# Kernel optimization log

Measured on AMD Instinct MI355X. Metric: run time of the kernel, lower is better.

Reference implementation:

```python
import jax, jax.numpy as jnp
import numpy as np

P = 7            # POOL_SIZE
NUM_CLASSES = 20
STRIDE = 16      # FEATURE_STRIDE
SCALE = 1.0 / STRIDE
C_IN = 512
C_MID = 2 * C_IN
C_CLS = P * P * (NUM_CLASSES + 1)        # 1029
C_BOX = P * P * (NUM_CLASSES + 1) * 4    # 4116
H, W = 38, 50
K = 300
IMG_H, IMG_W = 600.0, 800.0


def conv1x1(w, b, x):
    # w: [Cout, Cin], b: [Cout], x: [Cin, H, W] -> ReLU(conv) (CNNBlock = Conv2d 1x1 + ReLU)
    return jax.nn.relu(jnp.einsum('oi,ihw->ohw', w, x) + b[:, None, None])


def ps_roi_pool(maps, rois_xyxy):
    # maps: [Ctot, H, W] with Ctot = Cout*P*P, channel index = (c*P + ph)*P + pw
    # rois_xyxy: [K, 4] (x1, y1, x2, y2) in image coords. torchvision PSRoIPool math.
    Ctot, h, w = maps.shape
    Cout = Ctot // (P * P)
    x1 = jnp.round(rois_xyxy[:, 0]) * SCALE
    y1 = jnp.round(rois_xyxy[:, 1]) * SCALE
    x2 = (jnp.round(rois_xyxy[:, 2]) + 1.0) * SCALE
    y2 = (jnp.round(rois_xyxy[:, 3]) + 1.0) * SCALE
    roi_w = jnp.maximum(x2 - x1, 0.1)
    roi_h = jnp.maximum(y2 - y1, 0.1)
    bin_w = roi_w / P
    bin_h = roi_h / P
    i = jnp.arange(P, dtype=maps.dtype)
    hs = jnp.clip(jnp.floor(y1[:, None] + bin_h[:, None] * i), 0.0, h)        # [K,P]
    he = jnp.clip(jnp.ceil(y1[:, None] + bin_h[:, None] * (i + 1.0)), 0.0, h)
    ws = jnp.clip(jnp.floor(x1[:, None] + bin_w[:, None] * i), 0.0, w)
    we = jnp.clip(jnp.ceil(x1[:, None] + bin_w[:, None] * (i + 1.0)), 0.0, w)
    hidx = jnp.arange(h, dtype=maps.dtype)
    widx = jnp.arange(w, dtype=maps.dtype)
    hmask = ((hidx >= hs[..., None]) & (hidx < he[..., None])).astype(maps.dtype)  # [K,P,H]
    wmask = ((widx >= ws[..., None]) & (widx < we[..., None])).astype(maps.dtype)  # [K,P,W]
    maps_r = maps.reshape(Cout, P, P, h, w)
    t = jnp.einsum('cijhw,kih->kcijw', maps_r, hmask)     # reduce over h
    s = jnp.einsum('kcijw,kjw->kcij', t, wmask)           # reduce over w -> [K,Cout,P,P]
    cnt = ((he - hs)[:, :, None] * (we - ws)[:, None, :])[:, None]  # [K,1,P,P]
    return jnp.where(cnt > 0, s / jnp.maximum(cnt, 1.0), 0.0)


def setup_inputs() -> dict:
    key = jax.random.key(0)
    ks = jax.random.split(key, 10)
    feature = jax.random.normal(ks[0], (C_IN, H, W), dtype=jnp.float32)
    # rois in (y1, x1, y2, x2) image coords, matching the column permute in forward
    ymin = jax.random.uniform(ks[1], (K,), minval=0.0, maxval=IMG_H - 32.0)
    xmin = jax.random.uniform(ks[2], (K,), minval=0.0, maxval=IMG_W - 32.0)
    yh = jax.random.uniform(ks[3], (K,), minval=16.0, maxval=256.0)
    xw = jax.random.uniform(ks[4], (K,), minval=16.0, maxval=256.0)
    ymax = jnp.minimum(ymin + yh, IMG_H - 1.0)
    xmax = jnp.minimum(xmin + xw, IMG_W - 1.0)
    rois = jnp.stack([ymin, xmin, ymax, xmax], axis=1)
    sd1 = 1.0 / np.sqrt(C_IN)
    sd2 = 1.0 / np.sqrt(C_MID)
    w_double = jax.random.normal(ks[5], (C_MID, C_IN), dtype=jnp.float32) * sd1
    b_double = jnp.zeros((C_MID,), dtype=jnp.float32)
    w_score = jax.random.normal(ks[6], (C_CLS, C_MID), dtype=jnp.float32) * sd2
    b_score = jnp.zeros((C_CLS,), dtype=jnp.float32)
    w_bbox = jax.random.normal(ks[7], (C_BOX, C_MID), dtype=jnp.float32) * sd2
    b_bbox = jnp.zeros((C_BOX,), dtype=jnp.float32)
    return {"feature": feature, "rois": rois,
            "w_double": w_double, "b_double": b_double,
            "w_score": w_score, "b_score": b_score,
            "w_bbox": w_bbox, "b_bbox": b_bbox}


def reference(feature, rois, w_double, b_double, w_score, b_score, w_bbox, b_bbox):
    feat2 = conv1x1(w_double, b_double, feature)               # [2C, H, W]
    # rois given as (y1,x1,y2,x2) -> (x1,y1,x2,y2), per xy_indices_and_rois permute
    rois_xyxy = rois[:, jnp.array([1, 0, 3, 2])]
    score_maps = conv1x1(w_score, b_score, feat2)              # [P*P*(NC+1), H, W]
    class_vote = ps_roi_pool(score_maps, rois_xyxy)            # [K, NC+1, P, P]
    predicted_roi_score = jnp.mean(class_vote, axis=(-2, -1))  # AvgPool2d(P) + squeeze -> [K, NC+1]
    bbox_maps = conv1x1(w_bbox, b_bbox, feat2)                 # [P*P*(NC+1)*4, H, W]
    bbox_vote = ps_roi_pool(bbox_maps, rois_xyxy)              # [K, 4*(NC+1), P, P]
    predicted_roi_offset = jnp.mean(bbox_vote, axis=(-2, -1))  # [K, 4*(NC+1)]
    return predicted_roi_score, predicted_roi_offset
```

## Files before the change

kernel.cpp:

```cpp
#include <hip/hip_runtime.h>
#include <hip/hip_bf16.h>

#define P 7
#define C_IN 512
#define C_MID 1024
#define C_CLS 1029
#define C_BOX 4116
#define FH 38
#define FW 50
#define NPIX 1900
#define KROIS 300
#define COUT_SCORE 21
#define COUT_BOX 84
#define NPAIRS (KROIS * (COUT_SCORE + COUT_BOX))

#define LDP 40

__device__ float g_featT [NPIX * C_IN];
__device__ float g_feat2T[NPIX * C_MID];
__device__ float g_score [C_CLS * NPIX];
__device__ float g_bbox  [C_BOX * NPIX];

typedef __attribute__((ext_vector_type(8))) short bf16x8;
typedef __attribute__((ext_vector_type(4))) float f32x4;

__device__ __forceinline__ unsigned short f2b(float x) {
    unsigned u = __float_as_uint(x);
    unsigned r = u + 0x7fffu + ((u >> 16) & 1u);
    return (unsigned short)(r >> 16);
}
__device__ __forceinline__ float b2f(unsigned short h) {
    return __uint_as_float((unsigned)h << 16);
}

__device__ __forceinline__ void split16(const float4* v,
                                        unsigned short* dsth, unsigned short* dstl) {
    unsigned hu[8], lu[8];
    #pragma unroll
    for (int q = 0; q < 4; ++q) {
        const float a0 = v[q].x, a1 = v[q].y, a2 = v[q].z, a3 = v[q].w;
        const unsigned short h0 = f2b(a0), h1 = f2b(a1), h2 = f2b(a2), h3 = f2b(a3);
        const unsigned short l0 = f2b(a0 - b2f(h0)), l1 = f2b(a1 - b2f(h1));
        const unsigned short l2 = f2b(a2 - b2f(h2)), l3 = f2b(a3 - b2f(h3));
        hu[q * 2 + 0] = (unsigned)h0 | ((unsigned)h1 << 16);
        hu[q * 2 + 1] = (unsigned)h2 | ((unsigned)h3 << 16);
        lu[q * 2 + 0] = (unsigned)l0 | ((unsigned)l1 << 16);
        lu[q * 2 + 1] = (unsigned)l2 | ((unsigned)l3 << 16);
    }
    reinterpret_cast<uint4*>(dsth)[0] = make_uint4(hu[0], hu[1], hu[2], hu[3]);
    reinterpret_cast<uint4*>(dsth)[1] = make_uint4(hu[4], hu[5], hu[6], hu[7]);
    reinterpret_cast<uint4*>(dstl)[0] = make_uint4(lu[0], lu[1], lu[2], lu[3]);
    reinterpret_cast<uint4*>(dstl)[1] = make_uint4(lu[4], lu[5], lu[6], lu[7]);
}

__global__ __launch_bounds__(256) void transpose_k(const float* __restrict__ in)
{
    __shared__ float t[32][33];
    const int n0 = blockIdx.x * 32;
    const int k0 = blockIdx.y * 32;
    const int tx = threadIdx.x & 31;
    const int ty = threadIdx.x >> 5;
    #pragma unroll
    for (int j = 0; j < 4; ++j) {
        const int kk = k0 + ty + j * 8;
        const int nn = n0 + tx;
        t[ty + j * 8][tx] = (nn < NPIX) ? in[kk * NPIX + nn] : 0.f;
    }
    __syncthreads();
    #pragma unroll
    for (int j = 0; j < 4; ++j) {
        const int nn = n0 + ty + j * 8;
        const int kk = k0 + tx;
        if (nn < NPIX) g_featT[(size_t)nn * C_IN + kk] = t[tx][ty + j * 8];
    }
}

template <bool TROUT>
__global__ __launch_bounds__(256) void gemm_mfma(
    const float* __restrict__ W, const float* __restrict__ X,
    const float* __restrict__ bias, float* __restrict__ out,
    int M, int K, int N)
{
    __shared__ unsigned short sAh[128 * LDP], sAl[128 * LDP];
    __shared__ unsigned short sBh[128 * LDP], sBl[128 * LDP];

    const int tid = threadIdx.x;
    const int bm = blockIdx.y * 128;
    const int bn = blockIdx.x * 128;
    const int lane = tid & 63;
    const int wid = tid >> 6;
    const int wr = (wid >> 1) * 64;
    const int wc = (wid & 1) * 64;
    const int ll  = lane & 15;
    const int lh8 = (lane >> 4) * 8;
    const int lh4 = (lane >> 4) * 4;

    const int srow  = tid >> 1;
    const int skseg = (tid & 1) * 16;
    const int arow = bm + srow;
    const int brow = bn + srow;

    f32x4 acc[4][4];
    #pragma unroll
    for (int i = 0; i < 4; ++i)
        #pragma unroll
        for (int j = 0; j < 4; ++j) {
            f32x4 z = {0.f, 0.f, 0.f, 0.f};
            acc[i][j] = z;
        }

    float4 wa[4], wb[4];
    const float4 f4z = make_float4(0.f, 0.f, 0.f, 0.f);

    {
        const float* pa = W + (size_t)arow * K + skseg;
        if (arow < M) { wa[0] = ((const float4*)pa)[0]; wa[1] = ((const float4*)pa)[1];
                        wa[2] = ((const float4*)pa)[2]; wa[3] = ((const float4*)pa)[3]; }
        else          { wa[0] = wa[1] = wa[2] = wa[3] = f4z; }
        const float* pb = X + (size_t)brow * K + skseg;
        if (brow < N) { wb[0] = ((const float4*)pb)[0]; wb[1] = ((const float4*)pb)[1];
                        wb[2] = ((const float4*)pb)[2]; wb[3] = ((const float4*)pb)[3]; }
        else          { wb[0] = wb[1] = wb[2] = wb[3] = f4z; }
    }

    for (int k0 = 0; k0 < K; k0 += 32) {
        split16(wa, &sAh[srow * LDP + skseg], &sAl[srow * LDP + skseg]);
        split16(wb, &sBh[srow * LDP + skseg], &sBl[srow * LDP + skseg]);
        __syncthreads();

        const int kn = k0 + 32;
        if (kn < K) {
            const float* pa = W + (size_t)arow * K + kn + skseg;
            if (arow < M) { wa[0] = ((const float4*)pa)[0]; wa[1] = ((const float4*)pa)[1];
                            wa[2] = ((const float4*)pa)[2]; wa[3] = ((const float4*)pa)[3]; }
            const float* pb = X + (size_t)brow * K + kn + skseg;
            if (brow < N) { wb[0] = ((const float4*)pb)[0]; wb[1] = ((const float4*)pb)[1];
                            wb[2] = ((const float4*)pb)[2]; wb[3] = ((const float4*)pb)[3]; }
        }

        bf16x8 bhf[4], blf[4];
        #pragma unroll
        for (int nt = 0; nt < 4; ++nt) {
            const int r = wc + nt * 16 + ll;
            bhf[nt] = *reinterpret_cast<const bf16x8*>(&sBh[r * LDP + lh8]);
            blf[nt] = *reinterpret_cast<const bf16x8*>(&sBl[r * LDP + lh8]);
        }
        #pragma unroll
        for (int mt = 0; mt < 4; ++mt) {
            const int r = wr + mt * 16 + ll;
            const bf16x8 ahf = *reinterpret_cast<const bf16x8*>(&sAh[r * LDP + lh8]);
            const bf16x8 alf = *reinterpret_cast<const bf16x8*>(&sAl[r * LDP + lh8]);
            #pragma unroll
            for (int nt = 0; nt < 4; ++nt) {
                acc[mt][nt] = __builtin_amdgcn_mfma_f32_16x16x32_bf16(ahf, bhf[nt], acc[mt][nt], 0, 0, 0);
                acc[mt][nt] = __builtin_amdgcn_mfma_f32_16x16x32_bf16(ahf, blf[nt], acc[mt][nt], 0, 0, 0);
                acc[mt][nt] = __builtin_amdgcn_mfma_f32_16x16x32_bf16(alf, bhf[nt], acc[mt][nt], 0, 0, 0);
            }
        }
        __syncthreads();
    }

    #pragma unroll
    for (int mt = 0; mt < 4; ++mt) {
        #pragma unroll
        for (int nt = 0; nt < 4; ++nt) {
            const int m0 = bm + wr + mt * 16 + lh4;
            const int n  = bn + wc + nt * 16 + ll;
            if (TROUT) {
                if (n < N) {
                    float4 o;
                    o.x = fmaxf(acc[mt][nt][0] + bias[m0 + 0], 0.f);
                    o.y = fmaxf(acc[mt][nt][1] + bias[m0 + 1], 0.f);
                    o.z = fmaxf(acc[mt][nt][2] + bias[m0 + 2], 0.f);
                    o.w = fmaxf(acc[mt][nt][3] + bias[m0 + 3], 0.f);
                    *reinterpret_cast<float4*>(&out[(size_t)n * M + m0]) = o;
                }
            } else {
                #pragma unroll
                for (int r = 0; r < 4; ++r) {
                    const int m = m0 + r;
                    if (m < M && n < N)
                        out[(size_t)m * N + n] = fmaxf(acc[mt][nt][r] + bias[m], 0.f);
                }
            }
        }
    }
}

__global__ __launch_bounds__(256) void psroi_pool_mean(
    const float* __restrict__ rois, float* __restrict__ out)
{
    __shared__ float red[4][64];
    const int wid = threadIdx.x >> 6;
    const int lane = threadIdx.x & 63;
    const int pair = blockIdx.x * 4 + wid;

    const int k = pair / (COUT_SCORE + COUT_BOX);
    const int c = pair % (COUT_SCORE + COUT_BOX);

    const float* maps;
    int cbase;
    float* outp;
    if (c < COUT_SCORE) {
        maps = g_score;
        cbase = c * (P * P);
        outp = out + (size_t)k * COUT_SCORE + c;
    } else {
        const int cb = c - COUT_SCORE;
        maps = g_bbox;
        cbase = cb * (P * P);
        outp = out + (size_t)KROIS * COUT_SCORE + (size_t)k * COUT_BOX + cb;
    }

    const float ymin = rois[k * 4 + 0];
    const float xmin = rois[k * 4 + 1];
    const float ymax = rois[k * 4 + 2];
    const float xmax = rois[k * 4 + 3];

    const float x1 = __fmul_rn(rintf(xmin), 0.0625f);
    const float y1 = __fmul_rn(rintf(ymin), 0.0625f);
    const float x2 = __fmul_rn(__fadd_rn(rintf(xmax), 1.0f), 0.0625f);
    const float y2 = __fmul_rn(__fadd_rn(rintf(ymax), 1.0f), 0.0625f);
    const float roi_w = fmaxf(__fsub_rn(x2, x1), 0.1f);
    const float roi_h = fmaxf(__fsub_rn(y2, y1), 0.1f);
    const float inv7 = 1.0f / 7.0f;
    const float bin_w = __fmul_rn(roi_w, inv7);
    const float bin_h = __fmul_rn(roi_h, inv7);

    float val = 0.f;
    if (lane < P * P) {
        const int i = lane / P;
        const int j = lane % P;
        const float hs = fminf(fmaxf(floorf(__fadd_rn(y1, __fmul_rn(bin_h, (float)i))), 0.f), (float)FH);
        const float he = fminf(fmaxf(ceilf (__fadd_rn(y1, __fmul_rn(bin_h, (float)(i + 1)))), 0.f), (float)FH);
        const float wsb = fminf(fmaxf(floorf(__fadd_rn(x1, __fmul_rn(bin_w, (float)j))), 0.f), (float)FW);
        const float web = fminf(fmaxf(ceilf (__fadd_rn(x1, __fmul_rn(bin_w, (float)(j + 1)))), 0.f), (float)FW);
        const float cnt = __fmul_rn(__fsub_rn(he, hs), __fsub_rn(web, wsb));
        if (cnt > 0.f) {
            const int ys = (int)hs, ye = (int)he, xs = (int)wsb, xe = (int)web;
            const float* mp = maps + (size_t)(cbase + lane) * NPIX;
            float s = 0.f;
            for (int y = ys; y < ye; ++y)
                for (int x = xs; x < xe; ++x)
                    s += mp[y * FW + x];
            val = s / fmaxf(cnt, 1.0f);
        }
    }

    red[wid][lane] = val;
    __syncthreads();

    if (lane == 0) {
        float s = 0.f;
        for (int l = 0; l < P * P; ++l) s += red[wid][l];
        *outp = s * (1.0f / 49.0f);
    }
}

extern "C" void kernel_launch(void* const* d_in, const int* in_sizes, int n_in,
                              void* d_out, int out_size, void* d_ws, size_t ws_size,
                              hipStream_t stream) {
    const float* feature  = (const float*)d_in[0];
    const float* rois     = (const float*)d_in[1];
    const float* w_double = (const float*)d_in[2];
    const float* b_double = (const float*)d_in[3];
    const float* w_score  = (const float*)d_in[4];
    const float* b_score  = (const float*)d_in[5];
    const float* w_bbox   = (const float*)d_in[6];
    const float* b_bbox   = (const float*)d_in[7];
    float* out = (float*)d_out;

    float* featT  = nullptr; hipGetSymbolAddress((void**)&featT,  HIP_SYMBOL(g_featT));
    float* feat2T = nullptr; hipGetSymbolAddress((void**)&feat2T, HIP_SYMBOL(g_feat2T));
    float* scoreM = nullptr; hipGetSymbolAddress((void**)&scoreM, HIP_SYMBOL(g_score));
    float* bboxM  = nullptr; hipGetSymbolAddress((void**)&bboxM,  HIP_SYMBOL(g_bbox));

    const dim3 blk(256);

    transpose_k<<<dim3((NPIX + 31) / 32, C_IN / 32), blk, 0, stream>>>(feature);

    gemm_mfma<true ><<<dim3((NPIX + 127) / 128, (C_MID + 127) / 128), blk, 0, stream>>>(
        w_double, featT, b_double, feat2T, C_MID, C_IN, NPIX);

    gemm_mfma<false><<<dim3((NPIX + 127) / 128, (C_CLS + 127) / 128), blk, 0, stream>>>(
        w_score, feat2T, b_score, scoreM, C_CLS, C_MID, NPIX);
    gemm_mfma<false><<<dim3((NPIX + 127) / 128, (C_BOX + 127) / 128), blk, 0, stream>>>(
        w_bbox, feat2T, b_bbox, bboxM, C_BOX, C_MID, NPIX);

    psroi_pool_mean<<<dim3(NPAIRS / 4), blk, 0, stream>>>(rois, out);
}
```

Before: 240.4 us.

## Pre-split operands to padded bf16 hi/lo buffers and load tiles via global_load_lds

Weights and activations are now split into bf16 high/low planes by separate pre-pass kernels, with the matrices padded so the GEMM needs no bounds checks. The GEMM loads these planes directly into a swizzled 64 KB LDS tile using global_load_lds with K-step 64, replacing the per-iteration fp32 load and split in registers. The first GEMM writes its output already split, and the pooling loop gets a fixed 4x4 unrolled fast path for small bins. This cuts conversion work inside the GEMM inner loop. In exchange it adds extra kernels and memory traffic to re-split the weights on every call, and the load/compute overlap from register prefetching is lost.

Measured after the change: 218.4 us. -9.2%, faster.

```diff
diff --git a/kernel.cpp b/kernel.cpp
--- a/kernel.cpp
+++ b/kernel.cpp
@@ -14,12 +14,18 @@
 #define COUT_BOX 84
 #define NPAIRS (KROIS * (COUT_SCORE + COUT_BOX))
 
-#define LDP 40
-
-__device__ float g_featT [NPIX * C_IN];
-__device__ float g_feat2T[NPIX * C_MID];
-__device__ float g_score [C_CLS * NPIX];
-__device__ float g_bbox  [C_BOX * NPIX];
+#define MP1 1024
+#define MP2 1152
+#define MP3 4224
+#define NPAD 1920
+
+__device__ unsigned short g_w1h[MP1 * C_IN],  g_w1l[MP1 * C_IN];
+__device__ unsigned short g_w2h[MP2 * C_MID], g_w2l[MP2 * C_MID];
+__device__ unsigned short g_w3h[MP3 * C_MID], g_w3l[MP3 * C_MID];
+__device__ unsigned short g_fTh[NPAD * C_IN], g_fTl[NPAD * C_IN];
+__device__ unsigned short g_f2Th[NPAD * C_MID], g_f2Tl[NPAD * C_MID];
+__device__ float g_score[C_CLS * NPIX];
+__device__ float g_bbox [C_BOX * NPIX];
 
 typedef __attribute__((ext_vector_type(8))) short bf16x8;
 typedef __attribute__((ext_vector_type(4))) float f32x4;
@@ -33,27 +39,30 @@
     return __uint_as_float((unsigned)h << 16);
 }
 
-__device__ __forceinline__ void split16(const float4* v,
-                                        unsigned short* dsth, unsigned short* dstl) {
-    unsigned hu[8], lu[8];
-    #pragma unroll
-    for (int q = 0; q < 4; ++q) {
-        const float a0 = v[q].x, a1 = v[q].y, a2 = v[q].z, a3 = v[q].w;
-        const unsigned short h0 = f2b(a0), h1 = f2b(a1), h2 = f2b(a2), h3 = f2b(a3);
-        const unsigned short l0 = f2b(a0 - b2f(h0)), l1 = f2b(a1 - b2f(h1));
-        const unsigned short l2 = f2b(a2 - b2f(h2)), l3 = f2b(a3 - b2f(h3));
-        hu[q * 2 + 0] = (unsigned)h0 | ((unsigned)h1 << 16);
-        hu[q * 2 + 1] = (unsigned)h2 | ((unsigned)h3 << 16);
-        lu[q * 2 + 0] = (unsigned)l0 | ((unsigned)l1 << 16);
-        lu[q * 2 + 1] = (unsigned)l2 | ((unsigned)l3 << 16);
-    }
-    reinterpret_cast<uint4*>(dsth)[0] = make_uint4(hu[0], hu[1], hu[2], hu[3]);
-    reinterpret_cast<uint4*>(dsth)[1] = make_uint4(hu[4], hu[5], hu[6], hu[7]);
-    reinterpret_cast<uint4*>(dstl)[0] = make_uint4(lu[0], lu[1], lu[2], lu[3]);
-    reinterpret_cast<uint4*>(dstl)[1] = make_uint4(lu[4], lu[5], lu[6], lu[7]);
-}
-
-__global__ __launch_bounds__(256) void transpose_k(const float* __restrict__ in)
+#define GLOAD16(gp, lp)                                                        \
+    __builtin_amdgcn_global_load_lds(                                          \
+        (const __attribute__((address_space(1))) void*)(gp),                   \
+        (__attribute__((address_space(3))) void*)(lp), 16, 0, 0)
+
+__global__ __launch_bounds__(256) void split_pad_k(
+    const float* __restrict__ src,
+    unsigned short* __restrict__ h, unsigned short* __restrict__ l,
+    int n_in4, int n_pad4)
+{
+    const int i = blockIdx.x * 256 + threadIdx.x;
+    if (i >= n_pad4) return;
+    float4 v = make_float4(0.f, 0.f, 0.f, 0.f);
+    if (i < n_in4) v = reinterpret_cast<const float4*>(src)[i];
+    ushort4 hh, lv;
+    hh.x = f2b(v.x); lv.x = f2b(v.x - b2f(hh.x));
+    hh.y = f2b(v.y); lv.y = f2b(v.y - b2f(hh.y));
+    hh.z = f2b(v.z); lv.z = f2b(v.z - b2f(hh.z));
+    hh.w = f2b(v.w); lv.w = f2b(v.w - b2f(hh.w));
+    reinterpret_cast<ushort4*>(h)[i] = hh;
+    reinterpret_cast<ushort4*>(l)[i] = lv;
+}
+
+__global__ __launch_bounds__(256) void transpose_split_k(const float* __restrict__ in)
 {
     __shared__ float t[32][33];
     const int n0 = blockIdx.x * 32;
@@ -71,34 +80,42 @@
     for (int j = 0; j < 4; ++j) {
         const int nn = n0 + ty + j * 8;
         const int kk = k0 + tx;
-        if (nn < NPIX) g_featT[(size_t)nn * C_IN + kk] = t[tx][ty + j * 8];
+        const float v = t[tx][ty + j * 8];
+        const unsigned short hh = f2b(v);
+        g_fTh[(size_t)nn * C_IN + kk] = hh;
+        g_fTl[(size_t)nn * C_IN + kk] = f2b(v - b2f(hh));
     }
 }
 
 template <bool TROUT>
 __global__ __launch_bounds__(256) void gemm_mfma(
-    const float* __restrict__ W, const float* __restrict__ X,
-    const float* __restrict__ bias, float* __restrict__ out,
+    const unsigned short* __restrict__ Ah, const unsigned short* __restrict__ Al,
+    const unsigned short* __restrict__ Bh, const unsigned short* __restrict__ Bl,
+    const float* __restrict__ bias,
+    float* __restrict__ out,
+    unsigned short* __restrict__ outh,
+    unsigned short* __restrict__ outl,
     int M, int K, int N)
 {
-    __shared__ unsigned short sAh[128 * LDP], sAl[128 * LDP];
-    __shared__ unsigned short sBh[128 * LDP], sBl[128 * LDP];
+    __shared__ unsigned char lds[65536];
 
     const int tid = threadIdx.x;
     const int bm = blockIdx.y * 128;
     const int bn = blockIdx.x * 128;
     const int lane = tid & 63;
     const int wid = tid >> 6;
+    const int uwid = __builtin_amdgcn_readfirstlane(wid);
     const int wr = (wid >> 1) * 64;
     const int wc = (wid & 1) * 64;
-    const int ll  = lane & 15;
-    const int lh8 = (lane >> 4) * 8;
-    const int lh4 = (lane >> 4) * 4;
-
-    const int srow  = tid >> 1;
-    const int skseg = (tid & 1) * 16;
-    const int arow = bm + srow;
-    const int brow = bn + srow;
+    const int ll = lane & 15;
+    const int lg = lane >> 4;
+    const int lh4 = lg * 4;
+
+    const int lrow = lane >> 3;
+    const int lseg = (lane & 7) ^ lrow;
+    const unsigned short* gsrc = (uwid == 0) ? Ah : (uwid == 1) ? Al : (uwid == 2) ? Bh : Bl;
+    const int rbase = (uwid < 2) ? bm : bn;
+    unsigned char* lplane = &lds[uwid * 16384];
 
     f32x4 acc[4][4];
     #pragma unroll
@@ -109,52 +126,42 @@
             acc[i][j] = z;
         }
 
-    float4 wa[4], wb[4];
-    const float4 f4z = make_float4(0.f, 0.f, 0.f, 0.f);
-
-    {
-        const float* pa = W + (size_t)arow * K + skseg;
-        if (arow < M) { wa[0] = ((const float4*)pa)[0]; wa[1] = ((const float4*)pa)[1];
-                        wa[2] = ((const float4*)pa)[2]; wa[3] = ((const float4*)pa)[3]; }
-        else          { wa[0] = wa[1] = wa[2] = wa[3] = f4z; }
-        const float* pb = X + (size_t)brow * K + skseg;
-        if (brow < N) { wb[0] = ((const float4*)pb)[0]; wb[1] = ((const float4*)pb)[1];
-                        wb[2] = ((const float4*)pb)[2]; wb[3] = ((const float4*)pb)[3]; }
-        else          { wb[0] = wb[1] = wb[2] = wb[3] = f4z; }
-    }
-
-    for (int k0 = 0; k0 < K; k0 += 32) {
-        split16(wa, &sAh[srow * LDP + skseg], &sAl[srow * LDP + skseg]);
-        split16(wb, &sBh[srow * LDP + skseg], &sBl[srow * LDP + skseg]);
+    const unsigned char* pAh = &lds[0];
+    const unsigned char* pAl = &lds[16384];
+    const unsigned char* pBh = &lds[32768];
+    const unsigned char* pBl = &lds[49152];
+
+    for (int k0 = 0; k0 < K; k0 += 64) {
+        const unsigned short* gp = gsrc + (size_t)(rbase + lrow) * K + lseg * 8 + k0;
+        #pragma unroll
+        for (int g = 0; g < 16; ++g)
+            GLOAD16(gp + (size_t)g * 8 * K, lplane + g * 1024);
+        asm volatile("s_waitcnt vmcnt(0)" ::: "memory");
         __syncthreads();
 
-        const int kn = k0 + 32;
-        if (kn < K) {
-            const float* pa = W + (size_t)arow * K + kn + skseg;
-            if (arow < M) { wa[0] = ((const float4*)pa)[0]; wa[1] = ((const float4*)pa)[1];
-                            wa[2] = ((const float4*)pa)[2]; wa[3] = ((const float4*)pa)[3]; }
-            const float* pb = X + (size_t)brow * K + kn + skseg;
-            if (brow < N) { wb[0] = ((const float4*)pb)[0]; wb[1] = ((const float4*)pb)[1];
-                            wb[2] = ((const float4*)pb)[2]; wb[3] = ((const float4*)pb)[3]; }
-        }
-
-        bf16x8 bhf[4], blf[4];
         #pragma unroll
-        for (int nt = 0; nt < 4; ++nt) {
-            const int r = wc + nt * 16 + ll;
-            bhf[nt] = *reinterpret_cast<const bf16x8*>(&sBh[r * LDP + lh8]);
-            blf[nt] = *reinterpret_cast<const bf16x8*>(&sBl[r * LDP + lh8]);
-        }
-        #pragma unroll
-        for (int mt = 0; mt < 4; ++mt) {
-            const int r = wr + mt * 16 + ll;
-            const bf16x8 ahf = *reinterpret_cast<const bf16x8*>(&sAh[r * LDP + lh8]);
-            const bf16x8 alf = *reinterpret_cast<const bf16x8*>(&sAl[r * LDP + lh8]);
+        for (int kh = 0; kh < 2; ++kh) {
+            const int slot = kh * 4 + lg;
+            bf16x8 bh[4], bl[4];
             #pragma unroll
             for (int nt = 0; nt < 4; ++nt) {
-                acc[mt][nt] = __builtin_amdgcn_mfma_f32_16x16x32_bf16(ahf, bhf[nt], acc[mt][nt], 0, 0, 0);
-                acc[mt][nt] = __builtin_amdgcn_mfma_f32_16x16x32_bf16(ahf, blf[nt], acc[mt][nt], 0, 0, 0);
-                acc[mt][nt] = __builtin_amdgcn_mfma_f32_16x16x32_bf16(alf, bhf[nt], acc[mt][nt], 0, 0, 0);
+                const int r = wc + nt * 16 + ll;
+                const int so = ((slot ^ (r & 7)) << 4);
+                bh[nt] = *reinterpret_cast<const bf16x8*>(pBh + r * 128 + so);
+                bl[nt] = *reinterpret_cast<const bf16x8*>(pBl + r * 128 + so);
+            }
+            #pragma unroll
+            for (int mt = 0; mt < 4; ++mt) {
+                const int r = wr + mt * 16 + ll;
+                const int so = ((slot ^ (r & 7)) << 4);
+                const bf16x8 ah = *reinterpret_cast<const bf16x8*>(pAh + r * 128 + so);
+                const bf16x8 al = *reinterpret_cast<const bf16x8*>(pAl + r * 128 + so);
+                #pragma unroll
+                for (int nt = 0; nt < 4; ++nt) {
+                    acc[mt][nt] = __builtin_amdgcn_mfma_f32_16x16x32_bf16(ah, bh[nt], acc[mt][nt], 0, 0, 0);
+                    acc[mt][nt] = __builtin_amdgcn_mfma_f32_16x16x32_bf16(ah, bl[nt], acc[mt][nt], 0, 0, 0);
+                    acc[mt][nt] = __builtin_amdgcn_mfma_f32_16x16x32_bf16(al, bh[nt], acc[mt][nt], 0, 0, 0);
+                }
             }
         }
         __syncthreads();
@@ -167,14 +174,17 @@
             const int m0 = bm + wr + mt * 16 + lh4;
             const int n  = bn + wc + nt * 16 + ll;
             if (TROUT) {
-                if (n < N) {
-                    float4 o;
-                    o.x = fmaxf(acc[mt][nt][0] + bias[m0 + 0], 0.f);
-                    o.y = fmaxf(acc[mt][nt][1] + bias[m0 + 1], 0.f);
-                    o.z = fmaxf(acc[mt][nt][2] + bias[m0 + 2], 0.f);
-                    o.w = fmaxf(acc[mt][nt][3] + bias[m0 + 3], 0.f);
-                    *reinterpret_cast<float4*>(&out[(size_t)n * M + m0]) = o;
-                }
+                float o0 = fmaxf(acc[mt][nt][0] + bias[m0 + 0], 0.f);
+                float o1 = fmaxf(acc[mt][nt][1] + bias[m0 + 1], 0.f);
+                float o2 = fmaxf(acc[mt][nt][2] + bias[m0 + 2], 0.f);
+                float o3 = fmaxf(acc[mt][nt][3] + bias[m0 + 3], 0.f);
+                ushort4 hh, lv;
+                hh.x = f2b(o0); lv.x = f2b(o0 - b2f(hh.x));
+                hh.y = f2b(o1); lv.y = f2b(o1 - b2f(hh.y));
+                hh.z = f2b(o2); lv.z = f2b(o2 - b2f(hh.z));
+                hh.w = f2b(o3); lv.w = f2b(o3 - b2f(hh.w));
+                *reinterpret_cast<ushort4*>(&outh[(size_t)n * M + m0]) = hh;
+                *reinterpret_cast<ushort4*>(&outl[(size_t)n * M + m0]) = lv;
             } else {
                 #pragma unroll
                 for (int r = 0; r < 4; ++r) {
@@ -238,11 +248,22 @@
         const float cnt = __fmul_rn(__fsub_rn(he, hs), __fsub_rn(web, wsb));
         if (cnt > 0.f) {
             const int ys = (int)hs, ye = (int)he, xs = (int)wsb, xe = (int)web;
+            const int rows = ye - ys, cols = xe - xs;
             const float* mp = maps + (size_t)(cbase + lane) * NPIX;
             float s = 0.f;
-            for (int y = ys; y < ye; ++y)
-                for (int x = xs; x < xe; ++x)
-                    s += mp[y * FW + x];
+            if (rows <= 4 && cols <= 4) {
+                #pragma unroll
+                for (int t = 0; t < 16; ++t) {
+                    const int dy = t >> 2, dx = t & 3;
+                    const float v = (dy < rows && dx < cols)
+                                        ? mp[(ys + dy) * FW + (xs + dx)] : 0.f;
+                    s += v;
+                }
+            } else {
+                for (int y = ys; y < ye; ++y)
+                    for (int x = xs; x < xe; ++x)
+                        s += mp[y * FW + x];
+            }
             val = s / fmaxf(cnt, 1.0f);
         }
     }
@@ -270,22 +291,39 @@
     const float* b_bbox   = (const float*)d_in[7];
     float* out = (float*)d_out;
 
-    float* featT  = nullptr; hipGetSymbolAddress((void**)&featT,  HIP_SYMBOL(g_featT));
-    float* feat2T = nullptr; hipGetSymbolAddress((void**)&feat2T, HIP_SYMBOL(g_feat2T));
-    float* scoreM = nullptr; hipGetSymbolAddress((void**)&scoreM, HIP_SYMBOL(g_score));
-    float* bboxM  = nullptr; hipGetSymbolAddress((void**)&bboxM,  HIP_SYMBOL(g_bbox));
+    unsigned short *w1h, *w1l, *w2h, *w2l, *w3h, *w3l, *fTh, *fTl, *f2Th, *f2Tl;
+    float *scoreM, *bboxM;
+    hipGetSymbolAddress((void**)&w1h,  HIP_SYMBOL(g_w1h));
+    hipGetSymbolAddress((void**)&w1l,  HIP_SYMBOL(g_w1l));
+    hipGetSymbolAddress((void**)&w2h,  HIP_SYMBOL(g_w2h));
+    hipGetSymbolAddress((void**)&w2l,  HIP_SYMBOL(g_w2l));
+    hipGetSymbolAddress((void**)&w3h,  HIP_SYMBOL(g_w3h));
+    hipGetSymbolAddress((void**)&w3l,  HIP_SYMBOL(g_w3l));
+    hipGetSymbolAddress((void**)&fTh,  HIP_SYMBOL(g_fTh));
+    hipGetSymbolAddress((void**)&fTl,  HIP_SYMBOL(g_fTl));
+    hipGetSymbolAddress((void**)&f2Th, HIP_SYMBOL(g_f2Th));
+    hipGetSymbolAddress((void**)&f2Tl, HIP_SYMBOL(g_f2Tl));
+    hipGetSymbolAddress((void**)&scoreM, HIP_SYMBOL(g_score));
+    hipGetSymbolAddress((void**)&bboxM,  HIP_SYMBOL(g_bbox));
 
     const dim3 blk(256);
 
-    transpose_k<<<dim3((NPIX + 31) / 32, C_IN / 32), blk, 0, stream>>>(feature);
-
-    gemm_mfma<true ><<<dim3((NPIX + 127) / 128, (C_MID + 127) / 128), blk, 0, stream>>>(
-        w_double, featT, b_double, feat2T, C_MID, C_IN, NPIX);
-
-    gemm_mfma<false><<<dim3((NPIX + 127) / 128, (C_CLS + 127) / 128), blk, 0, stream>>>(
-        w_score, feat2T, b_score, scoreM, C_CLS, C_MID, NPIX);
-    gemm_mfma<false><<<dim3((NPIX + 127) / 128, (C_BOX + 127) / 128), blk, 0, stream>>>(
-        w_bbox, feat2T, b_bbox, bboxM, C_BOX, C_MID, NPIX);
+    split_pad_k<<<(MP1 * C_IN / 4 + 255) / 256, blk, 0, stream>>>(
+        w_double, w1h, w1l, C_MID * C_IN / 4, MP1 * C_IN / 4);
+    split_pad_k<<<(MP2 * C_MID / 4 + 255) / 256, blk, 0, stream>>>(
+        w_score, w2h, w2l, C_CLS * C_MID / 4, MP2 * C_MID / 4);
+    split_pad_k<<<(MP3 * C_MID / 4 + 255) / 256, blk, 0, stream>>>(
+        w_bbox, w3h, w3l, C_BOX * C_MID / 4, MP3 * C_MID / 4);
+
+    transpose_split_k<<<dim3(NPAD / 32, C_IN / 32), blk, 0, stream>>>(feature);
+
+    gemm_mfma<true ><<<dim3(NPAD / 128, MP1 / 128), blk, 0, stream>>>(
+        w1h, w1l, fTh, fTl, b_double, nullptr, f2Th, f2Tl, C_MID, C_IN, NPIX);
+
+    gemm_mfma<false><<<dim3(NPAD / 128, MP2 / 128), blk, 0, stream>>>(
+        w2h, w2l, f2Th, f2Tl, b_score, scoreM, nullptr, nullptr, C_CLS, C_MID, NPIX);
+    gemm_mfma<false><<<dim3(NPAD / 128, MP3 / 128), blk, 0, stream>>>(
+        w3h, w3l, f2Th, f2Tl, b_bbox, bboxM, nullptr, nullptr, C_BOX, C_MID, NPIX);
 
     psroi_pool_mean<<<dim3(NPAIRS / 4), blk, 0, stream>>>(rois, out);
 }
```
